# Performance work log

Hardware: AMD Instinct MI355X
Metric: run time of the kernel (lower is better)

## Reference

```python
import jax, jax.numpy as jnp
import numpy as np

NQ = 20
P_MAX = 480 * 640 - 1  # hardcoded clamp in original module


def make_quantizer_params(nq=NQ, mn=0.0, mx=1.0):
    # Replicates APLoss.__init__ conv1d weight/bias initialization.
    a = (nq - 1) / (mx - mn)
    w = np.concatenate([-a * np.ones(nq), a * np.ones(nq)]).astype(np.float32)
    b = np.concatenate([a * mn + np.arange(nq, 0, -1),
                        np.arange(2 - nq, 2, 1) - a * mn]).astype(np.float32)
    w[0] = w[-1] = 0.0
    b[0] = b[-1] = 1.0
    return jnp.asarray(w), jnp.asarray(b)


def setup_inputs() -> dict:
    key = jax.random.key(0)
    k1, k2, k3, k4, k5 = jax.random.split(key, 5)
    P, D, N, NEG = 307200, 64, 20000, 80
    qw, qb = make_quantizer_params()
    return {
        "descriptors1": jax.random.normal(k1, (1, P, D), dtype=jnp.float32),
        "descriptors2": jax.random.normal(k2, (1, P, D), dtype=jnp.float32),
        "qw": qw,
        "qb": qb,
        "matches_1": jax.random.randint(k3, (N,), 0, P),
        "matches_2": jax.random.randint(k4, (N,), 0, P),
        "offsets": jax.random.randint(k5, (NEG,), 0, 640),
    }


def reference(descriptors1, descriptors2, qw, qb, matches_1, matches_2, offsets):
    nq = qw.shape[0] // 2
    d1 = descriptors1[0]  # (P, D)
    d2 = descriptors2[0]  # (P, D)

    # negative indices: offset positive matches, clamp to valid pixel range
    non_m2 = jnp.clip(matches_2[:, None] + offsets[None, :], 0, P_MAX)  # (N, NEG)

    a1 = d1[matches_1]                                  # (N, D)
    pos = jnp.sum(a1 * d2[matches_2], axis=-1)          # (N,)
    neg = jnp.einsum('nd,nmd->nm', a1, d2[non_m2])      # (N, NEG)

    scores = jnp.concatenate([pos[:, None], neg], axis=1)   # (N, M), M = 1+NEG
    label = jnp.zeros_like(scores).at[:, 0].set(1.0)         # (N, M)

    # soft quantizer: 1x1 conv == per-bin affine; min of two halves, relu
    x = scores[:, None, :]                                   # (N, 1, M)
    q = jnp.minimum(qw[:nq, None] * x + qb[:nq, None],
                    qw[nq:, None] * x + qb[nq:, None])
    q = jnp.maximum(q, 0.0)                                  # (N, nq, M)

    nbs = q.sum(axis=-1)                                     # (N, nq)
    rec = (q * label[:, None, :]).sum(axis=-1)               # (N, nq)
    prec = jnp.cumsum(rec, axis=-1) / (1e-16 + jnp.cumsum(nbs, axis=-1))
    rec = rec / rec.sum(axis=-1, keepdims=True)
    ap = (prec * rec).sum(axis=-1)                           # (N,)
    return (1.0 - ap).mean()
```

## Files before the change

### kernel.cpp

```cpp
#include <hip/hip_runtime.h>

#define DIM 64
#define MAXBUCK 2560
#define SORT_T 1024

__global__ __launch_bounds__(1024) void k_sort(const int* __restrict__ m1,
                                               const int* __restrict__ m2,
                                               int* __restrict__ i1s,
                                               int* __restrict__ i2s,
                                               int N, int nbuck)
{
    __shared__ int cnt[MAXBUCK];
    __shared__ int s[SORT_T];
    const int tid = threadIdx.x;

    for (int i = tid; i < nbuck; i += SORT_T) cnt[i] = 0;
    __syncthreads();
    for (int i = tid; i < N; i += SORT_T) atomicAdd(&cnt[m2[i] >> 7], 1);
    __syncthreads();

    const int base = tid * 3;
    int loc[3];
    int sum = 0;
    #pragma unroll
    for (int u = 0; u < 3; ++u) {
        const int idx = base + u;
        const int v = (idx < nbuck) ? cnt[idx] : 0;
        loc[u] = sum;
        sum += v;
    }
    s[tid] = sum;
    __syncthreads();
    for (int off = 1; off < SORT_T; off <<= 1) {
        const int v = (tid >= off) ? s[tid - off] : 0;
        __syncthreads();
        s[tid] += v;
        __syncthreads();
    }
    const int excl = (tid > 0) ? s[tid - 1] : 0;
    #pragma unroll
    for (int u = 0; u < 3; ++u) {
        const int idx = base + u;
        if (idx < nbuck) cnt[idx] = excl + loc[u];
    }
    __syncthreads();
    for (int i = tid; i < N; i += SORT_T) {
        const int pos = atomicAdd(&cnt[m2[i] >> 7], 1);
        i1s[pos] = m1[i];
        i2s[pos] = m2[i];
    }
}

__global__ __launch_bounds__(256) void pixel_ap_main(
    const float* __restrict__ d1, const float* __restrict__ d2,
    const float* __restrict__ qw, const float* __restrict__ qb,
    const int* __restrict__ offs,
    const int* __restrict__ i1s, const int* __restrict__ i2s,
    float* __restrict__ partial, int P, int NEG, int NQ2, int N)
{
    const int tid = threadIdx.x;
    const int nq  = NQ2 >> 1;
    const int M   = NEG + 1;

    __shared__ float s_scores[96];
    __shared__ float s_red[4];

    const int b   = blockIdx.x;
    const int per = gridDim.x >> 3;
    const int pos = (b & 7) * per + (b >> 3);
    if (pos >= N) return;

    const int i1 = i1s[pos];
    const int i2 = i2s[pos];

    const int g  = tid >> 3;
    const int sl = tid & 7;

    int rows[3];
    #pragma unroll
    for (int t = 0; t < 3; ++t) {
        const int j = g + 32 * t;
        if (j < M) rows[t] = (j == 0) ? i2 : min(i2 + offs[j - 1], P - 1);
    }

    const float* a_ptr = d1 + (size_t)i1 * DIM + 8 * sl;
    const float4 a0 = ((const float4*)a_ptr)[0];
    const float4 a1 = ((const float4*)a_ptr)[1];

    float4 b0[3], b1[3];
    #pragma unroll
    for (int t = 0; t < 3; ++t) {
        const int j = g + 32 * t;
        if (j < M) {
            const float* p = d2 + (size_t)rows[t] * DIM + 8 * sl;
            b0[t] = ((const float4*)p)[0];
            b1[t] = ((const float4*)p)[1];
        }
    }
    #pragma unroll
    for (int t = 0; t < 3; ++t) {
        const int j = g + 32 * t;
        if (j < M) {
            float sd = b0[t].x * a0.x + b0[t].y * a0.y + b0[t].z * a0.z + b0[t].w * a0.w
                     + b1[t].x * a1.x + b1[t].y * a1.y + b1[t].z * a1.z + b1[t].w * a1.w;
            sd += __shfl_xor(sd, 1);
            sd += __shfl_xor(sd, 2);
            sd += __shfl_xor(sd, 4);
            if (sl == 0) s_scores[j] = sd;
        }
    }
    __syncthreads();
    if (tid >= 128) return;

    const float a_scale = qw[nq];
    const float amn     = qb[nq - 1] - 1.0f;
    const float ulim    = (float)(nq - 1);

    const float xp = s_scores[0];
    const float up = fminf(fmaxf(a_scale * xp - amn, 0.0f), ulim);
    const float ip = floorf(up);
    const float fp = up - ip;

    float n1 = 0.0f, n2 = 0.0f;
    if (tid < M) {
        const float x  = s_scores[tid];
        const float u  = fminf(fmaxf(a_scale * x - amn, 0.0f), ulim);
        const float fi = floorf(u);
        const float f  = u - fi;
        n2 = (fi >= ip)        ? 1.0f : ((fi == ip - 1.0f) ? f : 0.0f);
        n1 = (fi >= ip + 1.0f) ? 1.0f : ((fi == ip)        ? f : 0.0f);
    }
    #pragma unroll
    for (int off = 32; off >= 1; off >>= 1) {
        n1 += __shfl_xor(n1, off);
        n2 += __shfl_xor(n2, off);
    }
    const int wid = tid >> 6;
    if ((tid & 63) == 0) { s_red[wid] = n1; s_red[2 + wid] = n2; }
    __syncthreads();
    if (tid == 0) {
        const float N1 = s_red[0] + s_red[1];
        const float N2 = s_red[2] + s_red[3];
        const float ap = fp * fp / (1e-16f + N1) + (1.0f - fp) / (1e-16f + N2);
        partial[pos] = 1.0f - ap;
    }
}

__global__ __launch_bounds__(1024) void k_reduce(const float* __restrict__ partial,
                                                 float* __restrict__ out, int N)
{
    float s = 0.0f;
    for (int i = threadIdx.x; i < N; i += 1024) s += partial[i];
    #pragma unroll
    for (int off = 32; off >= 1; off >>= 1) s += __shfl_xor(s, off);
    __shared__ float sw[16];
    if ((threadIdx.x & 63) == 0) sw[threadIdx.x >> 6] = s;
    __syncthreads();
    if (threadIdx.x == 0) {
        float t = 0.0f;
        #pragma unroll
        for (int w = 0; w < 16; ++w) t += sw[w];
        out[0] = t / (float)N;
    }
}

extern "C" void kernel_launch(void* const* d_in, const int* in_sizes, int n_in,
                              void* d_out, int out_size, void* d_ws, size_t ws_size,
                              hipStream_t stream) {
    const float* d1   = (const float*)d_in[0];
    const float* d2   = (const float*)d_in[1];
    const float* qw   = (const float*)d_in[2];
    const float* qb   = (const float*)d_in[3];
    const int*   m1   = (const int*)d_in[4];
    const int*   m2   = (const int*)d_in[5];
    const int*   offs = (const int*)d_in[6];

    const int N     = in_sizes[4];
    const int P     = in_sizes[0] / DIM;
    const int NEG   = in_sizes[6];
    const int NQ2   = in_sizes[2];
    const int nbuck = (P + 127) >> 7;

    int*   i1s     = (int*)d_ws;
    int*   i2s     = i1s + N;
    float* partial = (float*)(i2s + N);

    k_sort<<<1, SORT_T, 0, stream>>>(m1, m2, i1s, i2s, N, nbuck);

    const int per = (N + 7) / 8;
    pixel_ap_main<<<8 * per, 256, 0, stream>>>(d1, d2, qw, qb, offs, i1s, i2s,
                                               partial, P, NEG, NQ2, N);

    k_reduce<<<1, 1024, 0, stream>>>(partial, (float*)d_out, N);
}
```

Baseline: 246.9 us.

## Split single-block bucket sort into multi-block histogram, scan and scatter kernels

```diff
diff --git a/kernel.cpp b/kernel.cpp
--- a/kernel.cpp
+++ b/kernel.cpp
@@ -1,29 +1,22 @@
 #include <hip/hip_runtime.h>
 
 #define DIM 64
-#define MAXBUCK 2560
-#define SORT_T 1024
-
-__global__ __launch_bounds__(1024) void k_sort(const int* __restrict__ m1,
-                                               const int* __restrict__ m2,
-                                               int* __restrict__ i1s,
-                                               int* __restrict__ i2s,
-                                               int N, int nbuck)
-{
-    __shared__ int cnt[MAXBUCK];
-    __shared__ int s[SORT_T];
-    const int tid = threadIdx.x;
-
-    for (int i = tid; i < nbuck; i += SORT_T) cnt[i] = 0;
-    __syncthreads();
-    for (int i = tid; i < N; i += SORT_T) atomicAdd(&cnt[m2[i] >> 7], 1);
-    __syncthreads();
-
-    const int base = tid * 3;
-    int loc[3];
+
+
+__global__ __launch_bounds__(256) void k_hist(const int* __restrict__ m2,
+                                              int* __restrict__ cnt, int N) {
+    const int i = blockIdx.x * 256 + threadIdx.x;
+    if (i < N) atomicAdd(&cnt[m2[i] >> 7], 1);
+}
+
+__global__ __launch_bounds__(256) void k_scan(int* __restrict__ cnt, int nbuck) {
+    __shared__ int s[256];
+    const int tid  = threadIdx.x;
+    const int base = tid * 10;
+    int loc[10];
     int sum = 0;
     #pragma unroll
-    for (int u = 0; u < 3; ++u) {
+    for (int u = 0; u < 10; ++u) {
         const int idx = base + u;
         const int v = (idx < nbuck) ? cnt[idx] : 0;
         loc[u] = sum;
@@ -31,7 +24,7 @@
     }
     s[tid] = sum;
     __syncthreads();
-    for (int off = 1; off < SORT_T; off <<= 1) {
+    for (int off = 1; off < 256; off <<= 1) {
         const int v = (tid >= off) ? s[tid - off] : 0;
         __syncthreads();
         s[tid] += v;
@@ -39,15 +32,23 @@
     }
     const int excl = (tid > 0) ? s[tid - 1] : 0;
     #pragma unroll
-    for (int u = 0; u < 3; ++u) {
+    for (int u = 0; u < 10; ++u) {
         const int idx = base + u;
         if (idx < nbuck) cnt[idx] = excl + loc[u];
     }
-    __syncthreads();
-    for (int i = tid; i < N; i += SORT_T) {
-        const int pos = atomicAdd(&cnt[m2[i] >> 7], 1);
+}
+
+__global__ __launch_bounds__(256) void k_scatter(const int* __restrict__ m1,
+                                                 const int* __restrict__ m2,
+                                                 int* __restrict__ cnt,
+                                                 int* __restrict__ i1s,
+                                                 int* __restrict__ i2s, int N) {
+    const int i = blockIdx.x * 256 + threadIdx.x;
+    if (i < N) {
+        const int v2  = m2[i];
+        const int pos = atomicAdd(&cnt[v2 >> 7], 1);
         i1s[pos] = m1[i];
-        i2s[pos] = m2[i];
+        i2s[pos] = v2;
     }
 }
 
@@ -181,11 +182,17 @@
     const int NQ2   = in_sizes[2];
     const int nbuck = (P + 127) >> 7;
 
-    int*   i1s     = (int*)d_ws;
+    int*   cnt     = (int*)d_ws;
+    int*   i1s     = cnt + nbuck;
     int*   i2s     = i1s + N;
     float* partial = (float*)(i2s + N);
 
-    k_sort<<<1, SORT_T, 0, stream>>>(m1, m2, i1s, i2s, N, nbuck);
+    const int nblk = (N + 255) / 256;
+
+    hipMemsetAsync(cnt, 0, (size_t)nbuck * sizeof(int), stream);
+    k_hist   <<<nblk, 256, 0, stream>>>(m2, cnt, N);
+    k_scan   <<<1, 256, 0, stream>>>(cnt, nbuck);
+    k_scatter<<<nblk, 256, 0, stream>>>(m1, m2, cnt, i1s, i2s, N);
 
     const int per = (N + 7) / 8;
     pixel_ap_main<<<8 * per, 256, 0, stream>>>(d1, d2, qw, qb, offs, i1s, i2s,
```

Result: faster. 202.8 us (-17.9%).
